# Performance work log

Measured on AMD Instinct MI355X. Metric: run time of the kernel, lower is better.

The kernel has to match this reference:

```python
import jax, jax.numpy as jnp
import numpy as np

B, L, D_MODEL, N_HEADS = 2, 2048, 2048, 16
HALF = D_MODEL // 2            # 1024
HD = HALF // N_HEADS           # 64 (head dim actually used by the reshape)
SCALE = float(np.sqrt(D_MODEL / N_HEADS))  # sqrt(128), per source's self.scale
EPS = 1e-5


def setup_inputs() -> dict:
    key = jax.random.key(0)
    ks = jax.random.split(key, 12)
    s = 1.0 / np.sqrt(HALF)
    d = dict(
        x_a=jax.random.normal(ks[0], (B, L, HALF), jnp.float32),
        x_b=jax.random.normal(ks[1], (B, L, HALF), jnp.float32),
        Wq_a=jax.random.normal(ks[2], (HALF, HALF), jnp.float32) * s,
        Wq_b=jax.random.normal(ks[3], (HALF, HALF), jnp.float32) * s,
        Wk_a=jax.random.normal(ks[4], (HALF, HALF), jnp.float32) * s,
        Wk_b=jax.random.normal(ks[5], (HALF, HALF), jnp.float32) * s,
        Wv_a=jax.random.normal(ks[6], (HALF, HALF), jnp.float32) * s,
        Wv_b=jax.random.normal(ks[7], (HALF, HALF), jnp.float32) * s,
        Wo_a=jax.random.normal(ks[8], (HALF, HALF), jnp.float32) * s,
        Wo_b=jax.random.normal(ks[9], (HALF, HALF), jnp.float32) * s,
        gamma_a=jnp.ones((HALF,), jnp.float32),
        beta_a=jnp.zeros((HALF,), jnp.float32),
        gamma_b=jnp.ones((HALF,), jnp.float32),
        beta_b=jnp.zeros((HALF,), jnp.float32),
    )
    return d


def _heads(x, W):
    # torch Linear (no bias): x @ W.T, then split heads -> (B, H, L, HD)
    y = jnp.einsum('bld,ed->ble', x, W)
    Bb, Ll, _ = y.shape
    return y.reshape(Bb, Ll, N_HEADS, HD).transpose(0, 2, 1, 3)


def _ln(x, gamma, beta):
    mu = jnp.mean(x, axis=-1, keepdims=True)
    var = jnp.var(x, axis=-1, keepdims=True)
    return (x - mu) * jax.lax.rsqrt(var + EPS) * gamma + beta


def reference(x_a, x_b, Wq_a, Wq_b, Wk_a, Wk_b, Wv_a, Wv_b, Wo_a, Wo_b,
              gamma_a, beta_a, gamma_b, beta_b):
    q_a = _heads(x_a, Wq_a); k_a = _heads(x_a, Wk_a); v_a = _heads(x_a, Wv_a)
    q_b = _heads(x_b, Wq_b); k_b = _heads(x_b, Wk_b); v_b = _heads(x_b, Wv_b)

    # cross-attention: branch a attends over branch b and vice versa
    scores_a = jnp.einsum('bhqd,bhkd->bhqk', q_a, k_b) / SCALE
    scores_b = jnp.einsum('bhqd,bhkd->bhqk', q_b, k_a) / SCALE
    w_a = jax.nn.softmax(scores_a, axis=-1)
    w_b = jax.nn.softmax(scores_b, axis=-1)

    o_a = jnp.einsum('bhqk,bhkd->bhqd', w_a, v_b)
    o_b = jnp.einsum('bhqk,bhkd->bhqd', w_b, v_a)
    o_a = o_a.transpose(0, 2, 1, 3).reshape(x_a.shape)
    o_b = o_b.transpose(0, 2, 1, 3).reshape(x_b.shape)

    o_a = jnp.einsum('bld,ed->ble', o_a, Wo_a)
    o_b = jnp.einsum('bld,ed->ble', o_b, Wo_b)

    y_a = _ln(x_a + o_a, gamma_a, beta_a)
    y_b = _ln(x_b + o_b, gamma_b, beta_b)
    return y_a, y_b
```

## Files before the change

### kernel.cpp

```cpp
#include <hip/hip_runtime.h>
#include <cstdint>
#include <cstddef>

typedef __bf16 bf16x8 __attribute__((ext_vector_type(8)));
typedef float f32x4 __attribute__((ext_vector_type(4)));
typedef unsigned short u16x8 __attribute__((ext_vector_type(8)));
typedef unsigned short u16x4 __attribute__((ext_vector_type(4)));
typedef short s16x4 __attribute__((ext_vector_type(4)));
typedef unsigned short u16;

#define L_SEQ 2048
#define D_HALF 1024
#define HDIM 64
static constexpr float EXP2_SCALE = 0.12751742552639395f;

__device__ inline u16 f2b(float f) {
  uint32_t u; __builtin_memcpy(&u, &f, 4);
  u = u + 0x7FFFu + ((u >> 16) & 1u);
  return (u16)(u >> 16);
}

__device__ inline uint32_t cvt_pk_bf16(float lo, float hi) {
  uint32_t r;
  asm("v_cvt_pk_bf16_f32 %0, %1, %2" : "=v"(r) : "v"(lo), "v"(hi));
  return r;
}

#define GLOAD16(gp, lp) __builtin_amdgcn_global_load_lds( \
    (const __attribute__((address_space(1))) unsigned int*)(gp), \
    (__attribute__((address_space(3))) unsigned int*)(lp), 16, 0, 0)

struct CArgAll { const float* src[10]; u16* dst[10]; };
__global__ __launch_bounds__(256)
void convall(CArgAll a) {
  const int id = blockIdx.x;
  const float* s; u16* d; int blk;
  if (id < 4096) { int p = id >> 11; blk = id & 2047; s = a.src[p]; d = a.dst[p]; }
  else { int w = (id - 4096) >> 9; blk = (id - 4096) & 511; s = a.src[2 + w]; d = a.dst[2 + w]; }
  size_t i = ((size_t)blk * 256 + threadIdx.x) * 8;
  float4 v0 = *(const float4*)(s + i);
  float4 v1 = *(const float4*)(s + i + 4);
  u16x8 p;
  p[0] = f2b(v0.x); p[1] = f2b(v0.y); p[2] = f2b(v0.z); p[3] = f2b(v0.w);
  p[4] = f2b(v1.x); p[5] = f2b(v1.y); p[6] = f2b(v1.z); p[7] = f2b(v1.w);
  *(u16x8*)&d[i] = p;
}

struct GArg { const u16* A; const u16* W; u16* C; const float* R; float* Z;
              int vt; float alpha; };
struct GArgs { GArg g[6]; };

template <bool RESID>
__global__ __launch_bounds__(256)
void gemm_nt(GArgs args, int N, int K, int ZN) {
  const int nwg = gridDim.x;
  const int q8 = nwg >> 3;
  const int bid = ((int)blockIdx.x & 7) * q8 + ((int)blockIdx.x >> 3);
  const int z = bid % ZN;
  const int rem = bid / ZN;
  const int nx = N >> 7;
  const int bx = rem % nx, by = rem / nx;

  GArg ga = args.g[z];
  __shared__ __attribute__((aligned(16))) u16 As[8192];
  __shared__ __attribute__((aligned(16))) u16 Bs[8192];

  const int tid = threadIdx.x;
  const int wv = tid >> 6, lane = tid & 63;
  const int lane15 = lane & 15, quad = lane >> 4;
  const int m0 = by * 128, n0 = bx * 128;
  const int wm = (wv >> 1) * 64, wn = (wv & 1) * 64;

  const int srow = lane >> 3;
  const int scol = ((lane & 7) ^ srow) * 8;

  const u16* pA[4]; const u16* pW[4]; int lo[4];
#pragma unroll
  for (int j = 0; j < 4; j++) {
    int r = wv * 32 + j * 8;
    pA[j] = ga.A + (size_t)(m0 + r + srow) * K + scol;
    pW[j] = ga.W + (size_t)(n0 + r + srow) * K + scol;
    lo[j] = r * 64;
  }

  f32x4 acc[4][4] = {};
  const int swz = (lane15 & 7) << 4;

  for (int k0 = 0; k0 < K; k0 += 64) {
    __syncthreads();
#pragma unroll
    for (int j = 0; j < 4; j++) {
      GLOAD16(pA[j] + k0, &As[lo[j]]);
      GLOAD16(pW[j] + k0, &Bs[lo[j]]);
    }
    __syncthreads();
    const char* ab = (const char*)As;
    const char* bb = (const char*)Bs;
#pragma unroll
    for (int kk = 0; kk < 2; kk++) {
      const int cb = kk * 64 + quad * 16;
      bf16x8 af[4], bw[4];
#pragma unroll
      for (int i = 0; i < 4; i++)
        af[i] = *(const bf16x8*)(ab + (wm + i * 16 + lane15) * 128 + (cb ^ swz));
#pragma unroll
      for (int j = 0; j < 4; j++)
        bw[j] = *(const bf16x8*)(bb + (wn + j * 16 + lane15) * 128 + (cb ^ swz));
#pragma unroll
      for (int i = 0; i < 4; i++)
#pragma unroll
        for (int j = 0; j < 4; j++)
          acc[i][j] = __builtin_amdgcn_mfma_f32_16x16x32_bf16(af[i], bw[j], acc[i][j], 0, 0, 0);
    }
  }

  const float al = ga.alpha;
  if (!RESID && ga.vt) {
#pragma unroll
    for (int i = 0; i < 4; i++)
#pragma unroll
      for (int j = 0; j < 4; j++) {
        int gm0 = m0 + wm + i * 16 + quad * 4;
        int gn  = n0 + wn + j * 16 + lane15;
        int bb2 = gm0 >> 11, tt = gm0 & 2047;
        u16x4 pk;
#pragma unroll
        for (int r = 0; r < 4; r++) pk[r] = f2b(acc[i][j][r] * al);
        *(u16x4*)&ga.C[(size_t)bb2 * 2097152 + (size_t)gn * 2048 + tt] = pk;
      }
  } else {
#pragma unroll
    for (int i = 0; i < 4; i++)
#pragma unroll
      for (int j = 0; j < 4; j++)
#pragma unroll
        for (int r = 0; r < 4; r++) {
          int gm = m0 + wm + i * 16 + quad * 4 + r;
          int gn = n0 + wn + j * 16 + lane15;
          size_t idx = (size_t)gm * N + gn;
          if (RESID) ga.Z[idx] = acc[i][j][r] + ga.R[idx];
          else       ga.C[idx] = f2b(acc[i][j][r] * al);
        }
  }
}

#define SWZ(row, bcol) ((row) * 128 + ((bcol) ^ (((row) & 7) << 4)))

__global__ __launch_bounds__(256, 2)
void attn_kernel(const u16* q_a, const u16* k_a, const u16* vt_a,
                 const u16* q_b, const u16* k_b, const u16* vt_b,
                 u16* o_a, u16* o_b) {
  const int br = blockIdx.z;
  const u16* Q  = br ? q_b : q_a;
  const u16* Kp = br ? k_a : k_b;
  const u16* Vp = br ? vt_a : vt_b;
  u16* O = br ? o_b : o_a;
  const int bh = blockIdx.y;
  const int b = bh >> 4, h = bh & 15;
  const int q0 = blockIdx.x * 128;

  const int tid = threadIdx.x, wv = tid >> 6, lane = tid & 63;
  const int lane15 = lane & 15, quad = lane >> 4;

  __shared__ __attribute__((aligned(16))) u16 Ks[2][4096];
  __shared__ __attribute__((aligned(16))) u16 Vt[2][4096];

  const size_t base   = ((size_t)b * L_SEQ) * D_HALF + (size_t)h * HDIM;
  const size_t vbase  = (size_t)b * 2097152 + (size_t)(h * 64) * 2048;

  const int c1 = tid + 256;
  const int r0 = tid >> 3, cb0 = (tid & 7) * 16;
  const int r1 = c1 >> 3,  cb1 = (c1 & 7) * 16;
  const int wo0 = SWZ(r0, cb0), wo1 = SWZ(r1, cb1);

  bf16x8 qf[2][2];
#pragma unroll
  for (int f = 0; f < 2; f++) {
    const int qrow = q0 + wv * 32 + f * 16 + lane15;
#pragma unroll
    for (int c = 0; c < 2; c++)
      qf[f][c] = *(const bf16x8*)&Q[base + (size_t)qrow * D_HALF + c * 32 + quad * 8];
  }

  u16x8 kr0 = *(const u16x8*)&Kp[base + (size_t)r0 * D_HALF + cb0 / 2];
  u16x8 kr1 = *(const u16x8*)&Kp[base + (size_t)r1 * D_HALF + cb1 / 2];
  u16x8 vr0 = *(const u16x8*)&Vp[vbase + (size_t)r0 * 2048 + cb0 / 2];
  u16x8 vr1 = *(const u16x8*)&Vp[vbase + (size_t)r1 * 2048 + cb1 / 2];
  *(u16x8*)((char*)Ks[0] + wo0) = kr0;
  *(u16x8*)((char*)Ks[0] + wo1) = kr1;
  *(u16x8*)((char*)Vt[0] + wo0) = vr0;
  *(u16x8*)((char*)Vt[0] + wo1) = vr1;
  __syncthreads();

  f32x4 oacc[2][4] = {};
  float lsum[2] = {0.f, 0.f};

  for (int it = 0; it < 32; it++) {
    const int cur = it & 1, nxt = cur ^ 1;
    if (it < 31) {
      const int kt = (it + 1) * 64;
      kr0 = *(const u16x8*)&Kp[base + (size_t)(kt + r0) * D_HALF + cb0 / 2];
      kr1 = *(const u16x8*)&Kp[base + (size_t)(kt + r1) * D_HALF + cb1 / 2];
      vr0 = *(const u16x8*)&Vp[vbase + (size_t)r0 * 2048 + kt + cb0 / 2];
      vr1 = *(const u16x8*)&Vp[vbase + (size_t)r1 * 2048 + kt + cb1 / 2];
    }

    const char* kb = (const char*)Ks[cur];
    const char* vb = (const char*)Vt[cur];

    f32x4 s[2][4];
    __builtin_amdgcn_s_setprio(1);
#pragma unroll
    for (int nt = 0; nt < 4; nt++) {
      const int krow = nt * 16 + lane15;
      bf16x8 kb0 = *(const bf16x8*)(kb + SWZ(krow, quad * 16));
      bf16x8 kb1 = *(const bf16x8*)(kb + SWZ(krow, 64 + quad * 16));
#pragma unroll
      for (int f = 0; f < 2; f++) {
        f32x4 a0 = {};
        a0 = __builtin_amdgcn_mfma_f32_16x16x32_bf16(kb0, qf[f][0], a0, 0, 0, 0);
        a0 = __builtin_amdgcn_mfma_f32_16x16x32_bf16(kb1, qf[f][1], a0, 0, 0, 0);
        s[f][nt] = a0;
      }
    }
    __builtin_amdgcn_s_setprio(0);

    s16x4 pa[2][4];
#pragma unroll
    for (int f = 0; f < 2; f++)
#pragma unroll
      for (int nt = 0; nt < 4; nt++) {
        float p0 = __builtin_amdgcn_exp2f(s[f][nt][0]);
        float p1 = __builtin_amdgcn_exp2f(s[f][nt][1]);
        float p2 = __builtin_amdgcn_exp2f(s[f][nt][2]);
        float p3 = __builtin_amdgcn_exp2f(s[f][nt][3]);
        lsum[f] += (p0 + p1) + (p2 + p3);
        union { uint32_t u[2]; s16x4 v; } cv;
        cv.u[0] = cvt_pk_bf16(p0, p1);
        cv.u[1] = cvt_pk_bf16(p2, p3);
        pa[f][nt] = cv.v;
      }

    __builtin_amdgcn_s_setprio(1);
#pragma unroll
    for (int dt = 0; dt < 4; dt++) {
      const int vrow = dt * 16 + lane15;
      s16x4 bv[4];
#pragma unroll
      for (int nt = 0; nt < 4; nt++)
        bv[nt] = *(const s16x4*)(vb + SWZ(vrow, nt * 32 + quad * 8));
#pragma unroll
      for (int f = 0; f < 2; f++) {
        f32x4 t = oacc[f][dt];
#pragma unroll
        for (int nt = 0; nt < 4; nt++)
          t = __builtin_amdgcn_mfma_f32_16x16x16bf16_1k(pa[f][nt], bv[nt], t, 0, 0, 0);
        oacc[f][dt] = t;
      }
    }
    __builtin_amdgcn_s_setprio(0);

    if (it < 31) {
      *(u16x8*)((char*)Ks[nxt] + wo0) = kr0;
      *(u16x8*)((char*)Ks[nxt] + wo1) = kr1;
      *(u16x8*)((char*)Vt[nxt] + wo0) = vr0;
      *(u16x8*)((char*)Vt[nxt] + wo1) = vr1;
    }
    __syncthreads();
  }

#pragma unroll
  for (int f = 0; f < 2; f++) {
    float lt = lsum[f];
    lt += __shfl_xor(lt, 16);
    lt += __shfl_xor(lt, 32);
    lsum[f] = lt;
  }
#pragma unroll
  for (int f = 0; f < 2; f++) {
    float linv[4];
#pragma unroll
    for (int r = 0; r < 4; r++)
      linv[r] = 1.0f / __shfl(lsum[f], quad * 4 + r);
#pragma unroll
    for (int dt = 0; dt < 4; dt++)
#pragma unroll
      for (int r = 0; r < 4; r++) {
        float val = oacc[f][dt][r] * linv[r];
        O[base + (size_t)(q0 + wv * 32 + f * 16 + quad * 4 + r) * D_HALF
          + dt * 16 + lane15] = f2b(val);
      }
  }
}

__global__ __launch_bounds__(256)
void ln_kernel(const float* zA, const float* zB,
               const float* gA, const float* bA, const float* gB, const float* bB,
               float* out) {
  const int row = blockIdx.x, br = blockIdx.y;
  const float* z = (br ? zB : zA) + (size_t)row * D_HALF;
  const float* g  = br ? gB : gA;
  const float* be = br ? bB : bA;
  float* o = out + (size_t)br * ((size_t)4096 * D_HALF) + (size_t)row * D_HALF;

  float4 v = ((const float4*)z)[threadIdx.x];
  float s  = v.x + v.y + v.z + v.w;
  float s2 = v.x * v.x + v.y * v.y + v.z * v.z + v.w * v.w;
#pragma unroll
  for (int off = 32; off > 0; off >>= 1) {
    s  += __shfl_down(s, off);
    s2 += __shfl_down(s2, off);
  }
  __shared__ float red[8];
  int w = threadIdx.x >> 6, ln = threadIdx.x & 63;
  if (ln == 0) { red[w] = s; red[4 + w] = s2; }
  __syncthreads();
  if (threadIdx.x == 0) {
    red[0] = red[0] + red[1] + red[2] + red[3];
    red[4] = red[4] + red[5] + red[6] + red[7];
  }
  __syncthreads();
  float mu  = red[0] * (1.0f / 1024.0f);
  float var = red[4] * (1.0f / 1024.0f) - mu * mu;
  float rs  = rsqrtf(fmaxf(var, 0.0f) + 1e-5f);

  int col = threadIdx.x * 4;
  float4 gv = ((const float4*)g)[threadIdx.x];
  float4 bv = ((const float4*)be)[threadIdx.x];
  float4 ov;
  ov.x = (v.x - mu) * rs * gv.x + bv.x;
  ov.y = (v.y - mu) * rs * gv.y + bv.y;
  ov.z = (v.z - mu) * rs * gv.z + bv.z;
  ov.w = (v.w - mu) * rs * gv.w + bv.w;
  *(float4*)&o[col] = ov;
}

extern "C" void kernel_launch(void* const* d_in, const int* in_sizes, int n_in,
                              void* d_out, int out_size, void* d_ws, size_t ws_size,
                              hipStream_t stream) {
  const float* x_a     = (const float*)d_in[0];
  const float* x_b     = (const float*)d_in[1];
  const float* Wq_a    = (const float*)d_in[2];
  const float* Wq_b    = (const float*)d_in[3];
  const float* Wk_a    = (const float*)d_in[4];
  const float* Wk_b    = (const float*)d_in[5];
  const float* Wv_a    = (const float*)d_in[6];
  const float* Wv_b    = (const float*)d_in[7];
  const float* Wo_a    = (const float*)d_in[8];
  const float* Wo_b    = (const float*)d_in[9];
  const float* gamma_a = (const float*)d_in[10];
  const float* beta_a  = (const float*)d_in[11];
  const float* gamma_b = (const float*)d_in[12];
  const float* beta_b  = (const float*)d_in[13];

  const size_t BUF = (size_t)4096 * 1024;
  u16* ws   = (u16*)d_ws;
  u16* q_a  = ws + 0 * BUF; u16* k_a  = ws + 1 * BUF; u16* vt_a = ws + 2 * BUF;
  u16* q_b  = ws + 3 * BUF; u16* k_b  = ws + 4 * BUF; u16* vt_b = ws + 5 * BUF;
  u16* wall = ws + 6 * BUF;
  float* z_a = (float*)(ws + 0 * BUF);
  float* z_b = (float*)(ws + 2 * BUF);

  u16* xbf_a = (u16*)d_out;
  u16* xbf_b = xbf_a + 4194304;
  u16* o_a   = (u16*)d_out;
  u16* o_b   = o_a + 4194304;

  const int N = 1024, K = 1024;

  CArgAll ca;
  ca.src[0] = x_a;  ca.dst[0] = xbf_a;
  ca.src[1] = x_b;  ca.dst[1] = xbf_b;
  ca.src[2] = Wq_a; ca.src[3] = Wk_a; ca.src[4] = Wv_a;
  ca.src[5] = Wq_b; ca.src[6] = Wk_b; ca.src[7] = Wv_b;
  ca.src[8] = Wo_a; ca.src[9] = Wo_b;
  for (int w = 0; w < 8; w++) ca.dst[2 + w] = wall + (size_t)w * 1048576;
  convall<<<dim3(8192), 256, 0, stream>>>(ca);

  GArgs qkv;
  qkv.g[0] = GArg{xbf_a, wall + 0 * 1048576, q_a,  nullptr, nullptr, 0, EXP2_SCALE};
  qkv.g[1] = GArg{xbf_a, wall + 1 * 1048576, k_a,  nullptr, nullptr, 0, 1.0f};
  qkv.g[2] = GArg{xbf_a, wall + 2 * 1048576, vt_a, nullptr, nullptr, 1, 1.0f};
  qkv.g[3] = GArg{xbf_b, wall + 3 * 1048576, q_b,  nullptr, nullptr, 0, EXP2_SCALE};
  qkv.g[4] = GArg{xbf_b, wall + 4 * 1048576, k_b,  nullptr, nullptr, 0, 1.0f};
  qkv.g[5] = GArg{xbf_b, wall + 5 * 1048576, vt_b, nullptr, nullptr, 1, 1.0f};
  gemm_nt<false><<<dim3(8 * 32 * 6), 256, 0, stream>>>(qkv, N, K, 6);

  attn_kernel<<<dim3(16, 32, 2), 256, 0, stream>>>(q_a, k_a, vt_a, q_b, k_b, vt_b, o_a, o_b);

  GArgs op;
  op.g[0] = GArg{o_a, wall + 6 * 1048576, nullptr, x_a, z_a, 0, 1.0f};
  op.g[1] = GArg{o_b, wall + 7 * 1048576, nullptr, x_b, z_b, 0, 1.0f};
  op.g[2] = op.g[0]; op.g[3] = op.g[0]; op.g[4] = op.g[0]; op.g[5] = op.g[0];
  gemm_nt<true><<<dim3(8 * 32 * 2), 256, 0, stream>>>(op, N, K, 2);

  ln_kernel<<<dim3(4096, 2), 256, 0, stream>>>(z_a, z_b, gamma_a, beta_a,
                                               gamma_b, beta_b, (float*)d_out);
}
```

Before: 341.7 us.

## Use direct global-to-LDS loads in attention and drop GEMM XCD block remapping

The attention kernel's K/V tile staging moves from register loads followed by LDS stores to direct global-to-LDS loads (GLOAD16) that write straight into the next double buffer. The explicit LDS write phase after compute goes away, which frees registers and lets the copies overlap compute without staging. Separately, the GEMM launch changes from a 1D grid with XCD-aware block remapping to a plain 3D grid, giving up the L2 locality that the remap was meant to provide. The direct loads rely on the GLOAD16 macro and a swizzled source address so the data lands in LDS in the layout the readers expect.

```diff
diff --git a/kernel.cpp b/kernel.cpp
--- a/kernel.cpp
+++ b/kernel.cpp
@@ -52,23 +52,15 @@
 
 template <bool RESID>
 __global__ __launch_bounds__(256)
-void gemm_nt(GArgs args, int N, int K, int ZN) {
-  const int nwg = gridDim.x;
-  const int q8 = nwg >> 3;
-  const int bid = ((int)blockIdx.x & 7) * q8 + ((int)blockIdx.x >> 3);
-  const int z = bid % ZN;
-  const int rem = bid / ZN;
-  const int nx = N >> 7;
-  const int bx = rem % nx, by = rem / nx;
-
-  GArg ga = args.g[z];
+void gemm_nt(GArgs args, int N, int K) {
+  GArg ga = args.g[blockIdx.z];
   __shared__ __attribute__((aligned(16))) u16 As[8192];
   __shared__ __attribute__((aligned(16))) u16 Bs[8192];
 
   const int tid = threadIdx.x;
   const int wv = tid >> 6, lane = tid & 63;
   const int lane15 = lane & 15, quad = lane >> 4;
-  const int m0 = by * 128, n0 = bx * 128;
+  const int m0 = blockIdx.y * 128, n0 = blockIdx.x * 128;
   const int wm = (wv >> 1) * 64, wn = (wv & 1) * 64;
 
   const int srow = lane >> 3;
@@ -168,10 +160,12 @@
   const size_t base   = ((size_t)b * L_SEQ) * D_HALF + (size_t)h * HDIM;
   const size_t vbase  = (size_t)b * 2097152 + (size_t)(h * 64) * 2048;
 
-  const int c1 = tid + 256;
-  const int r0 = tid >> 3, cb0 = (tid & 7) * 16;
-  const int r1 = c1 >> 3,  cb1 = (c1 & 7) * 16;
-  const int wo0 = SWZ(r0, cb0), wo1 = SWZ(r1, cb1);
+  const int lrow = lane >> 3;
+  const int sc  = ((lane & 7) ^ lrow) * 8;
+  const int row0 = wv * 8 + lrow;
+  const int row1 = 32 + wv * 8 + lrow;
+  const int ldo0 = (wv * 8) * 128;
+  const int ldo1 = (32 + wv * 8) * 128;
 
   bf16x8 qf[2][2];
 #pragma unroll
@@ -182,14 +176,10 @@
       qf[f][c] = *(const bf16x8*)&Q[base + (size_t)qrow * D_HALF + c * 32 + quad * 8];
   }
 
-  u16x8 kr0 = *(const u16x8*)&Kp[base + (size_t)r0 * D_HALF + cb0 / 2];
-  u16x8 kr1 = *(const u16x8*)&Kp[base + (size_t)r1 * D_HALF + cb1 / 2];
-  u16x8 vr0 = *(const u16x8*)&Vp[vbase + (size_t)r0 * 2048 + cb0 / 2];
-  u16x8 vr1 = *(const u16x8*)&Vp[vbase + (size_t)r1 * 2048 + cb1 / 2];
-  *(u16x8*)((char*)Ks[0] + wo0) = kr0;
-  *(u16x8*)((char*)Ks[0] + wo1) = kr1;
-  *(u16x8*)((char*)Vt[0] + wo0) = vr0;
-  *(u16x8*)((char*)Vt[0] + wo1) = vr1;
+  GLOAD16(Kp + base + (size_t)row0 * D_HALF + sc, (char*)Ks[0] + ldo0);
+  GLOAD16(Kp + base + (size_t)row1 * D_HALF + sc, (char*)Ks[0] + ldo1);
+  GLOAD16(Vp + vbase + (size_t)row0 * 2048 + sc,  (char*)Vt[0] + ldo0);
+  GLOAD16(Vp + vbase + (size_t)row1 * 2048 + sc,  (char*)Vt[0] + ldo1);
   __syncthreads();
 
   f32x4 oacc[2][4] = {};
@@ -199,10 +189,10 @@
     const int cur = it & 1, nxt = cur ^ 1;
     if (it < 31) {
       const int kt = (it + 1) * 64;
-      kr0 = *(const u16x8*)&Kp[base + (size_t)(kt + r0) * D_HALF + cb0 / 2];
-      kr1 = *(const u16x8*)&Kp[base + (size_t)(kt + r1) * D_HALF + cb1 / 2];
-      vr0 = *(const u16x8*)&Vp[vbase + (size_t)r0 * 2048 + kt + cb0 / 2];
-      vr1 = *(const u16x8*)&Vp[vbase + (size_t)r1 * 2048 + kt + cb1 / 2];
+      GLOAD16(Kp + base + (size_t)(kt + row0) * D_HALF + sc, (char*)Ks[nxt] + ldo0);
+      GLOAD16(Kp + base + (size_t)(kt + row1) * D_HALF + sc, (char*)Ks[nxt] + ldo1);
+      GLOAD16(Vp + vbase + (size_t)row0 * 2048 + kt + sc,    (char*)Vt[nxt] + ldo0);
+      GLOAD16(Vp + vbase + (size_t)row1 * 2048 + kt + sc,    (char*)Vt[nxt] + ldo1);
     }
 
     const char* kb = (const char*)Ks[cur];
@@ -260,12 +250,6 @@
     }
     __builtin_amdgcn_s_setprio(0);
 
-    if (it < 31) {
-      *(u16x8*)((char*)Ks[nxt] + wo0) = kr0;
-      *(u16x8*)((char*)Ks[nxt] + wo1) = kr1;
-      *(u16x8*)((char*)Vt[nxt] + wo0) = vr0;
-      *(u16x8*)((char*)Vt[nxt] + wo1) = vr1;
-    }
     __syncthreads();
   }
 
@@ -384,7 +368,7 @@
   qkv.g[3] = GArg{xbf_b, wall + 3 * 1048576, q_b,  nullptr, nullptr, 0, EXP2_SCALE};
   qkv.g[4] = GArg{xbf_b, wall + 4 * 1048576, k_b,  nullptr, nullptr, 0, 1.0f};
   qkv.g[5] = GArg{xbf_b, wall + 5 * 1048576, vt_b, nullptr, nullptr, 1, 1.0f};
-  gemm_nt<false><<<dim3(8 * 32 * 6), 256, 0, stream>>>(qkv, N, K, 6);
+  gemm_nt<false><<<dim3(8, 32, 6), 256, 0, stream>>>(qkv, N, K);
 
   attn_kernel<<<dim3(16, 32, 2), 256, 0, stream>>>(q_a, k_a, vt_a, q_b, k_b, vt_b, o_a, o_b);
 
@@ -392,7 +376,7 @@
   op.g[0] = GArg{o_a, wall + 6 * 1048576, nullptr, x_a, z_a, 0, 1.0f};
   op.g[1] = GArg{o_b, wall + 7 * 1048576, nullptr, x_b, z_b, 0, 1.0f};
   op.g[2] = op.g[0]; op.g[3] = op.g[0]; op.g[4] = op.g[0]; op.g[5] = op.g[0];
-  gemm_nt<true><<<dim3(8 * 32 * 2), 256, 0, stream>>>(op, N, K, 2);
+  gemm_nt<true><<<dim3(8, 32, 2), 256, 0, stream>>>(op, N, K);
 
   ln_kernel<<<dim3(4096, 2), 256, 0, stream>>>(z_a, z_b, gamma_a, beta_a,
                                                gamma_b, beta_b, (float*)d_out);
```

Result: faster. 326.1 us (-4.6%).
